# Kernel tuning notes

Measured on AMD Instinct MI355X. Metric: run time of the kernel, lower is better.

The kernel has to match this reference:

```python
import jax, jax.numpy as jnp
import numpy as np

T_STEPS = 200       # num_diffusion_steps
NUM_CLASSES = 21
PRECISION = 1e-4
EPS = 1e-10


def _alpha_cumprod(num_steps=T_STEPS, precision=PRECISION):
    steps = jnp.arange(num_steps + 1, dtype=jnp.float32) / num_steps
    ac = jnp.cos((steps + precision) / (1.0 + precision) * jnp.pi / 2.0) ** 2
    ac = ac / ac[0]
    betas = jnp.clip(1.0 - ac[1:] / ac[:-1], 0.0, 0.999)
    alphas = 1.0 - betas
    return jnp.cumprod(alphas)


def setup_inputs() -> dict:
    key = jax.random.key(0)
    k1, k2 = jax.random.split(key)
    B, S, C = 64, 4096, NUM_CLASSES
    x_0 = jax.random.uniform(k1, (B, S, C), dtype=jnp.float32)
    t = jax.random.randint(k2, (B,), 0, T_STEPS)
    return {"x_0": x_0, "t": t}


def reference(x_0, t):
    # q_sample(x_0, t, return_logits=True)
    B, S, C = x_0.shape
    alpha_t = _alpha_cumprod()[t]                     # [B]
    target = 1.0 / C                                   # uniform target distribution
    eye = jnp.eye(C, dtype=x_0.dtype)
    # transition matrix is constant over seq positions: [B, C, C]
    q_small = alpha_t[:, None, None] * eye + (1.0 - alpha_t)[:, None, None] * target
    log_q = jnp.log(q_small + EPS)                     # [B, C, C]
    # x_0^T @ log(q_t): contract over source class axis
    logits = jnp.einsum('bsc,bcd->bsd', x_0, log_q)    # [B, S, C]
    # module returns the full per-position transition tensor as well
    q_t = jnp.broadcast_to(q_small[:, None], (B, S, C, C))
    return logits, q_t
```

## Files before the change

kernel.cpp:

```cpp
#include <hip/hip_runtime.h>
#include <hip/hip_bf16.h>
#include <math.h>

#define NB 64
#define NS 4096
#define NC 21
#define NCC 441
#define TSTEPS 200

typedef float vfloat4 __attribute__((ext_vector_type(4)));


__global__ __launch_bounds__(64) void schedule_kernel(const int* __restrict__ t,
                                                      float4* __restrict__ ws) {
    int b = threadIdx.x;
    int tb = t[b];
    const float HPI = 1.5707963267948966f;
    const float P = 1e-4f;
    float cum = 1.0f;
    float alpha = 1.0f;
    float c0 = cosf(P / (1.0f + P) * HPI);
    for (int i = 0; i < TSTEPS; ++i) {
        float s1 = ((float)(i + 1) / (float)TSTEPS + P) / (1.0f + P) * HPI;
        float c1 = cosf(s1);
        float beta = 1.0f - (c1 * c1) / (c0 * c0);
        beta = fminf(fmaxf(beta, 0.0f), 0.999f);
        cum *= (1.0f - beta);
        if (i == tb) alpha = cum;
        c0 = c1;
    }
    float qo = (1.0f - alpha) / (float)NC;
    float qd = qo + alpha;
    float Loff  = logf(qo + 1e-10f);
    float Ldiag = logf(qd + 1e-10f);
    ws[b] = make_float4(qo, qd, Loff, Ldiag - Loff);
}

__global__ __launch_bounds__(256) void fused_kernel(const float* __restrict__ x0,
                                                    const float4* __restrict__ ws,
                                                    float* __restrict__ logits,
                                                    float* __restrict__ qt) {
    const int tid = threadIdx.x;
    const int id = blockIdx.x;
    const int div17 = id / 17;

    if (id % 17 != 0) {
        const int blk = id - 1 - div17;
        const int b = blk >> 8;
        const float4 w = ws[b];
        const float qo = w.x, qd = w.y;

        vfloat4* dst = (vfloat4*)qt + (size_t)blk * 1764;

        int p = tid * 4;
        if (p >= 882) p -= 882;
        else if (p >= 441) p -= 441;
        int r = p % 22;

#pragma unroll
        for (int k = 0; k < 7; ++k) {
            const int idx = tid + k * 256;
            vfloat4 v;
#pragma unroll
            for (int m = 0; m < 4; ++m) {
                const int pm = p + m;
                const int rm = r + m;
                const bool diag = (pm >= 441) ? (pm == 441) : (rm == 0 || rm == 22);
                v[m] = diag ? qd : qo;
            }
            if (idx < 1764) __builtin_nontemporal_store(v, &dst[idx]);
            p += 142; r += 10;
            if (p >= 441) { p -= 441; r -= 1; }
            if (r >= 22) r -= 22;
        }
    } else {
        __shared__ float4 s4[1344];
        const int blk = div17;
        const int b = blk >> 4;
        const float4 w = ws[b];
        const float Loff = w.z, Ldelta = w.w;

        const float4* g = (const float4*)x0 + (size_t)blk * 1344;
#pragma unroll
        for (int k = 0; k < 6; ++k) {
            int idx = tid + k * 256;
            if (idx < 1344) s4[idx] = g[idx];
        }
        __syncthreads();

        float* sf = (float*)s4;
        float x[NC];
        float S = 0.0f;
#pragma unroll
        for (int c = 0; c < NC; ++c) { x[c] = sf[tid * NC + c]; S += x[c]; }
        float base = Loff * S;
#pragma unroll
        for (int d = 0; d < NC; ++d) sf[tid * NC + d] = fmaf(Ldelta, x[d], base);
        __syncthreads();

        float4* o = (float4*)logits + (size_t)blk * 1344;
#pragma unroll
        for (int k = 0; k < 6; ++k) {
            int idx = tid + k * 256;
            if (idx < 1344) o[idx] = s4[idx];
        }
    }
}

extern "C" void kernel_launch(void* const* d_in, const int* in_sizes, int n_in,
                              void* d_out, int out_size, void* d_ws, size_t ws_size,
                              hipStream_t stream) {
    const float* x0 = (const float*)d_in[0];
    const int*   t  = (const int*)d_in[1];
    float* out    = (float*)d_out;
    float* logits = out;
    float* qt     = out + (size_t)NB * NS * NC;
    float4* ws    = (float4*)d_ws;

    schedule_kernel<<<1, 64, 0, stream>>>(t, ws);
    fused_kernel<<<17408, 256, 0, stream>>>(x0, ws, logits, qt);
}
```

Measured before the change: 530.8 us.

## Inline closed-form alpha schedule and make qt blocks write four tiles each

Drops the separate 200-step schedule kernel and instead computes alpha_cumprod per block in closed form from the cosine ratio, since the clipped cumulative product telescopes. This removes one launch and its serial dependency. The grid is split into 1024 logits blocks followed by 4096 qt blocks, each of which stores four identical 1764-vector tiles. The qt stores become plain rather than nontemporal. Risks are small numeric differences from __cosf and the telescoping shortcut, including the 0.999 beta clamp, which is only handled at the last step.

```diff
diff --git a/kernel.cpp b/kernel.cpp
--- a/kernel.cpp
+++ b/kernel.cpp
@@ -1,84 +1,64 @@
 #include <hip/hip_runtime.h>
-#include <hip/hip_bf16.h>
 #include <math.h>
 
 #define NB 64
 #define NS 4096
 #define NC 21
-#define NCC 441
-#define TSTEPS 200
 
 typedef float vfloat4 __attribute__((ext_vector_type(4)));
 
-
-__global__ __launch_bounds__(64) void schedule_kernel(const int* __restrict__ t,
-                                                      float4* __restrict__ ws) {
-    int b = threadIdx.x;
-    int tb = t[b];
-    const float HPI = 1.5707963267948966f;
-    const float P = 1e-4f;
-    float cum = 1.0f;
-    float alpha = 1.0f;
-    float c0 = cosf(P / (1.0f + P) * HPI);
-    for (int i = 0; i < TSTEPS; ++i) {
-        float s1 = ((float)(i + 1) / (float)TSTEPS + P) / (1.0f + P) * HPI;
-        float c1 = cosf(s1);
-        float beta = 1.0f - (c1 * c1) / (c0 * c0);
-        beta = fminf(fmaxf(beta, 0.0f), 0.999f);
-        cum *= (1.0f - beta);
-        if (i == tb) alpha = cum;
-        c0 = c1;
-    }
-    float qo = (1.0f - alpha) / (float)NC;
-    float qd = qo + alpha;
-    float Loff  = logf(qo + 1e-10f);
-    float Ldiag = logf(qd + 1e-10f);
-    ws[b] = make_float4(qo, qd, Loff, Ldiag - Loff);
-}
-
 __global__ __launch_bounds__(256) void fused_kernel(const float* __restrict__ x0,
-                                                    const float4* __restrict__ ws,
+                                                    const int* __restrict__ t,
                                                     float* __restrict__ logits,
                                                     float* __restrict__ qt) {
+    __shared__ float4 s4[1344];
     const int tid = threadIdx.x;
     const int id = blockIdx.x;
-    const int div17 = id / 17;
+    const bool is_log = (id < 1024);
+    const int b = is_log ? (id >> 4) : ((id - 1024) >> 6);
 
-    if (id % 17 != 0) {
-        const int blk = id - 1 - div17;
-        const int b = blk >> 8;
-        const float4 w = ws[b];
-        const float qo = w.x, qd = w.y;
+    const int tb = t[b];
+    const float K = 1.5707963267948966f / 1.0001f;
+    const int ti = (tb >= 199) ? 199 : (tb + 1);
+    const float c0 = __cosf(1e-4f * K);
+    const float c1 = __cosf(((float)ti * 0.005f + 1e-4f) * K);
+    float alpha = (c1 * c1) / (c0 * c0);
+    if (tb >= 199) alpha *= 0.001f;
+    const float qo = (1.0f - alpha) * (1.0f / 21.0f);
+    const float qd = qo + alpha;
 
-        vfloat4* dst = (vfloat4*)qt + (size_t)blk * 1764;
-
+    if (!is_log) {
+        const int qb = id - 1024;
         int p = tid * 4;
-        if (p >= 882) p -= 882;
-        else if (p >= 441) p -= 441;
+        if (p >= 882) p -= 882; else if (p >= 441) p -= 441;
         int r = p % 22;
-
+        vfloat4 vals[7];
 #pragma unroll
         for (int k = 0; k < 7; ++k) {
-            const int idx = tid + k * 256;
-            vfloat4 v;
 #pragma unroll
             for (int m = 0; m < 4; ++m) {
                 const int pm = p + m;
                 const int rm = r + m;
                 const bool diag = (pm >= 441) ? (pm == 441) : (rm == 0 || rm == 22);
-                v[m] = diag ? qd : qo;
+                vals[k][m] = diag ? qd : qo;
             }
-            if (idx < 1764) __builtin_nontemporal_store(v, &dst[idx]);
             p += 142; r += 10;
             if (p >= 441) { p -= 441; r -= 1; }
             if (r >= 22) r -= 22;
         }
+        vfloat4* dst = (vfloat4*)qt + (size_t)qb * (4 * 1764) + tid;
+#pragma unroll
+        for (int j = 0; j < 4; ++j) {
+#pragma unroll
+            for (int k = 0; k < 7; ++k) {
+                if (tid + k * 256 < 1764) dst[k * 256] = vals[k];
+            }
+            dst += 1764;
+        }
     } else {
-        __shared__ float4 s4[1344];
-        const int blk = div17;
-        const int b = blk >> 4;
-        const float4 w = ws[b];
-        const float Loff = w.z, Ldelta = w.w;
+        const float Loff   = logf(qo + 1e-10f);
+        const float Ldelta = logf(qd + 1e-10f) - Loff;
+        const int blk = id;
 
         const float4* g = (const float4*)x0 + (size_t)blk * 1344;
 #pragma unroll
@@ -93,7 +73,7 @@
         float S = 0.0f;
 #pragma unroll
         for (int c = 0; c < NC; ++c) { x[c] = sf[tid * NC + c]; S += x[c]; }
-        float base = Loff * S;
+        const float base = Loff * S;
 #pragma unroll
         for (int d = 0; d < NC; ++d) sf[tid * NC + d] = fmaf(Ldelta, x[d], base);
         __syncthreads();
@@ -115,8 +95,6 @@
     float* out    = (float*)d_out;
     float* logits = out;
     float* qt     = out + (size_t)NB * NS * NC;
-    float4* ws    = (float4*)d_ws;
 
-    schedule_kernel<<<1, 64, 0, stream>>>(t, ws);
-    fused_kernel<<<17408, 256, 0, stream>>>(x0, ws, logits, qt);
+    fused_kernel<<<5120, 256, 0, stream>>>(x0, t, logits, qt);
 }
```

After: 463.0 us. 1.15x faster.
